# Kernel tuning notes

Hardware: AMD Instinct MI355X
Metric: run time of the kernel (lower is better)

The kernel has to match this reference:

```python
import jax, jax.numpy as jnp
import numpy as np

N_ENTRIES = 4_194_304   # total CSR entries (gene observations)
H, W = 256, 256
N_PIXELS = H * W
N_GENES = 30000
FEATURE_DIM = 64


def setup_inputs() -> dict:
    key = jax.random.key(0)
    k1, k2, k3, k4 = jax.random.split(key, 4)
    # gene id per CSR entry
    indices = jax.random.randint(k1, (N_ENTRIES,), 0, N_GENES, dtype=jnp.int64)
    # counts per entry (positive floats)
    cnts = jax.random.uniform(k2, (N_ENTRIES,), dtype=jnp.float32) * 10.0
    # CSR row pointers over pixels: sorted, starting at 0, ending at N_ENTRIES
    indptr = jnp.sort(jax.random.randint(k3, (N_PIXELS + 1,), 0, N_ENTRIES + 1, dtype=jnp.int64))
    indptr = indptr.at[0].set(0).at[-1].set(N_ENTRIES)
    # params: gamma init zeros, tokens variance_scaling(1.0,'fan_in','normal',out_axis=0)
    gamma = jnp.zeros((N_GENES,), jnp.float32)
    tokens = jax.random.normal(k4, (N_GENES, FEATURE_DIM), dtype=jnp.float32) * (1.0 / np.sqrt(FEATURE_DIM))
    return {"indices": indices, "cnts": cnts, "indptr": indptr, "gamma": gamma, "tokens": tokens}


def reference(indices, cnts, indptr, gamma, tokens):
    # SGStem with rescale=True, normalize=False (module defaults)
    n_entries = indices.shape[0]
    n_pixels = indptr.shape[0] - 1  # == H*W
    # mask padding entries beyond indptr[-1]
    valid = jnp.arange(n_entries) < indptr[-1]
    c = jnp.where(valid, cnts, 0.0)
    # rescale counts by per-gene exp(gamma)
    c = c * jnp.exp(gamma[indices])
    # CSR -> segment ids per entry
    rpt = jnp.diff(indptr)
    segms = jnp.repeat(jnp.arange(n_pixels), rpt, total_repeat_length=n_entries)
    # gather token embeddings, scale, scatter-add into pixel bins
    embeddings = tokens[indices] * c[:, None]  # (n_entries, feature_dim)
    embedding_sum = jax.ops.segment_sum(embeddings, segms, num_segments=n_pixels)
    return embedding_sum.reshape(H, W, tokens.shape[-1])
```

## Files before the change

### kernel.cpp

```cpp
#include <hip/hip_runtime.h>
#include <hip/hip_bf16.h>

#define FDIM 64
#define N_PIXELS 65536
#define WAVES_PER_BLOCK 4

__global__ __launch_bounds__(WAVES_PER_BLOCK * 64) void sgstem_kernel(
    const int* __restrict__ indices,
    const float* __restrict__ cnts,
    const int* __restrict__ indptr,
    const float* __restrict__ gamma,
    const float4* __restrict__ tokens4,
    float4* __restrict__ out4)
{
    __shared__ int2 meta[WAVES_PER_BLOCK][64];

    const int lane = threadIdx.x & 63;
    const int wave = threadIdx.x >> 6;
    const int g    = lane >> 4;
    const int fl   = lane & 15;
    const int pixel = blockIdx.x * WAVES_PER_BLOCK + wave;

    const int start = indptr[pixel];
    const int end   = indptr[pixel + 1];

    float4 acc = {0.f, 0.f, 0.f, 0.f};

    for (int base = start; base < end; base += 64) {
        const int e = base + lane;
        int   idx   = 0;
        float scale = 0.0f;
        if (e < end) {
            idx   = indices[e];
            scale = cnts[e] * __expf(gamma[idx]);
        }
        int2 mt;
        mt.x = idx;
        mt.y = __float_as_int(scale);
        meta[wave][lane] = mt;

        const int m = end - base;
        if (m >= 64) {
            #pragma unroll 8
            for (int j = 0; j < 16; ++j) {
                const int2 mm = meta[wave][j * 4 + g];
                const float s = __int_as_float(mm.y);
                const float4 t = tokens4[mm.x * 16 + fl];
                acc.x = fmaf(t.x, s, acc.x);
                acc.y = fmaf(t.y, s, acc.y);
                acc.z = fmaf(t.z, s, acc.z);
                acc.w = fmaf(t.w, s, acc.w);
            }
        } else {
            const int niter = (m + 3) >> 2;
            for (int j = 0; j < niter; ++j) {
                const int2 mm = meta[wave][j * 4 + g];
                const float s = __int_as_float(mm.y);
                const float4 t = tokens4[mm.x * 16 + fl];
                acc.x = fmaf(t.x, s, acc.x);
                acc.y = fmaf(t.y, s, acc.y);
                acc.z = fmaf(t.z, s, acc.z);
                acc.w = fmaf(t.w, s, acc.w);
            }
        }
    }

    acc.x += __shfl_xor(acc.x, 16);
    acc.y += __shfl_xor(acc.y, 16);
    acc.z += __shfl_xor(acc.z, 16);
    acc.w += __shfl_xor(acc.w, 16);
    acc.x += __shfl_xor(acc.x, 32);
    acc.y += __shfl_xor(acc.y, 32);
    acc.z += __shfl_xor(acc.z, 32);
    acc.w += __shfl_xor(acc.w, 32);

    if (g == 0) {
        out4[pixel * 16 + fl] = acc;
    }
}

extern "C" void kernel_launch(void* const* d_in, const int* in_sizes, int n_in,
                              void* d_out, int out_size, void* d_ws, size_t ws_size,
                              hipStream_t stream) {
    const int*    indices = (const int*)d_in[0];
    const float*  cnts    = (const float*)d_in[1];
    const int*    indptr  = (const int*)d_in[2];
    const float*  gamma   = (const float*)d_in[3];
    const float4* tokens4 = (const float4*)d_in[4];
    float4*       out4    = (float4*)d_out;

    const int nblocks = N_PIXELS / WAVES_PER_BLOCK;
    sgstem_kernel<<<nblocks, WAVES_PER_BLOCK * 64, 0, stream>>>(
        indices, cnts, indptr, gamma, tokens4, out4);
}
```

Baseline: 178.2 us.

## Gather bf16 token table and process several pixels per wave

Adds a pre-pass kernel that converts the fp32 token table to bf16 in workspace. The main kernel then gathers 16-byte bf16 rows (8 lanes per entry, 8 entries per wave step) instead of fp32 rows, halving gather traffic per entry. Each wave now processes 8 pixels sequentially with a wider shuffle reduction. This gives up precision in the token values and adds an extra launch, and fewer waves may reduce latency hiding.

```diff
diff --git a/kernel.cpp b/kernel.cpp
--- a/kernel.cpp
+++ b/kernel.cpp
@@ -3,79 +3,119 @@
 
 #define FDIM 64
 #define N_PIXELS 65536
+#define N_GENES 30000
 #define WAVES_PER_BLOCK 4
+#define PIX_PER_WAVE 8
 
-__global__ __launch_bounds__(WAVES_PER_BLOCK * 64) void sgstem_kernel(
+__device__ __forceinline__ unsigned short f32_to_bf16_rne(float f) {
+    unsigned int u = __float_as_uint(f);
+    u = (u + 0x7FFFu + ((u >> 16) & 1u)) >> 16;
+    return (unsigned short)u;
+}
+
+__global__ __launch_bounds__(256) void convert_tokens(
+    const float4* __restrict__ tokens4,
+    ushort4* __restrict__ tok_bf)
+{
+    const int i = blockIdx.x * blockDim.x + threadIdx.x;
+    const float4 t = tokens4[i];
+    ushort4 o;
+    o.x = f32_to_bf16_rne(t.x);
+    o.y = f32_to_bf16_rne(t.y);
+    o.z = f32_to_bf16_rne(t.z);
+    o.w = f32_to_bf16_rne(t.w);
+    tok_bf[i] = o;
+}
+
+__global__ __launch_bounds__(WAVES_PER_BLOCK * 64) void sgstem_main(
     const int* __restrict__ indices,
     const float* __restrict__ cnts,
     const int* __restrict__ indptr,
     const float* __restrict__ gamma,
-    const float4* __restrict__ tokens4,
+    const uint4* __restrict__ tok_bf,
     float4* __restrict__ out4)
 {
     __shared__ int2 meta[WAVES_PER_BLOCK][64];
 
     const int lane = threadIdx.x & 63;
     const int wave = threadIdx.x >> 6;
-    const int g    = lane >> 4;
-    const int fl   = lane & 15;
-    const int pixel = blockIdx.x * WAVES_PER_BLOCK + wave;
+    const int g    = lane >> 3;
+    const int fl   = lane & 7;
+    const int wgid = blockIdx.x * WAVES_PER_BLOCK + wave;
+    const int p0   = wgid * PIX_PER_WAVE;
 
-    const int start = indptr[pixel];
-    const int end   = indptr[pixel + 1];
+    for (int pixel = p0; pixel < p0 + PIX_PER_WAVE; ++pixel) {
+        const int start = indptr[pixel];
+        const int end   = indptr[pixel + 1];
 
-    float4 acc = {0.f, 0.f, 0.f, 0.f};
+        float a0 = 0.f, a1 = 0.f, a2 = 0.f, a3 = 0.f;
+        float a4 = 0.f, a5 = 0.f, a6 = 0.f, a7 = 0.f;
 
-    for (int base = start; base < end; base += 64) {
-        const int e = base + lane;
-        int   idx   = 0;
-        float scale = 0.0f;
-        if (e < end) {
-            idx   = indices[e];
-            scale = cnts[e] * __expf(gamma[idx]);
-        }
-        int2 mt;
-        mt.x = idx;
-        mt.y = __float_as_int(scale);
-        meta[wave][lane] = mt;
+        for (int base = start; base < end; base += 64) {
+            const int e = base + lane;
+            int   idx   = 0;
+            float scale = 0.0f;
+            if (e < end) {
+                idx   = indices[e];
+                scale = cnts[e] * __expf(gamma[idx]);
+            }
+            int2 mt;
+            mt.x = idx;
+            mt.y = __float_as_int(scale);
+            meta[wave][lane] = mt;
 
-        const int m = end - base;
-        if (m >= 64) {
-            #pragma unroll 8
-            for (int j = 0; j < 16; ++j) {
-                const int2 mm = meta[wave][j * 4 + g];
-                const float s = __int_as_float(mm.y);
-                const float4 t = tokens4[mm.x * 16 + fl];
-                acc.x = fmaf(t.x, s, acc.x);
-                acc.y = fmaf(t.y, s, acc.y);
-                acc.z = fmaf(t.z, s, acc.z);
-                acc.w = fmaf(t.w, s, acc.w);
-            }
-        } else {
-            const int niter = (m + 3) >> 2;
-            for (int j = 0; j < niter; ++j) {
-                const int2 mm = meta[wave][j * 4 + g];
-                const float s = __int_as_float(mm.y);
-                const float4 t = tokens4[mm.x * 16 + fl];
-                acc.x = fmaf(t.x, s, acc.x);
-                acc.y = fmaf(t.y, s, acc.y);
-                acc.z = fmaf(t.z, s, acc.z);
-                acc.w = fmaf(t.w, s, acc.w);
+            const int m = end - base;
+            if (m >= 64) {
+                #pragma unroll 8
+                for (int j = 0; j < 8; ++j) {
+                    const int2 mm = meta[wave][j * 8 + g];
+                    const float s = __int_as_float(mm.y);
+                    const uint4 t = tok_bf[mm.x * 8 + fl];
+                    a0 = fmaf(__uint_as_float(t.x << 16), s, a0);
+                    a1 = fmaf(__uint_as_float(t.x & 0xFFFF0000u), s, a1);
+                    a2 = fmaf(__uint_as_float(t.y << 16), s, a2);
+                    a3 = fmaf(__uint_as_float(t.y & 0xFFFF0000u), s, a3);
+                    a4 = fmaf(__uint_as_float(t.z << 16), s, a4);
+                    a5 = fmaf(__uint_as_float(t.z & 0xFFFF0000u), s, a5);
+                    a6 = fmaf(__uint_as_float(t.w << 16), s, a6);
+                    a7 = fmaf(__uint_as_float(t.w & 0xFFFF0000u), s, a7);
+                }
+            } else {
+                const int niter = (m + 7) >> 3;
+                for (int j = 0; j < niter; ++j) {
+                    const int2 mm = meta[wave][j * 8 + g];
+                    const float s = __int_as_float(mm.y);
+                    const uint4 t = tok_bf[mm.x * 8 + fl];
+                    a0 = fmaf(__uint_as_float(t.x << 16), s, a0);
+                    a1 = fmaf(__uint_as_float(t.x & 0xFFFF0000u), s, a1);
+                    a2 = fmaf(__uint_as_float(t.y << 16), s, a2);
+                    a3 = fmaf(__uint_as_float(t.y & 0xFFFF0000u), s, a3);
+                    a4 = fmaf(__uint_as_float(t.z << 16), s, a4);
+                    a5 = fmaf(__uint_as_float(t.z & 0xFFFF0000u), s, a5);
+                    a6 = fmaf(__uint_as_float(t.w << 16), s, a6);
+                    a7 = fmaf(__uint_as_float(t.w & 0xFFFF0000u), s, a7);
+                }
             }
         }
-    }
 
-    acc.x += __shfl_xor(acc.x, 16);
-    acc.y += __shfl_xor(acc.y, 16);
-    acc.z += __shfl_xor(acc.z, 16);
-    acc.w += __shfl_xor(acc.w, 16);
-    acc.x += __shfl_xor(acc.x, 32);
-    acc.y += __shfl_xor(acc.y, 32);
-    acc.z += __shfl_xor(acc.z, 32);
-    acc.w += __shfl_xor(acc.w, 32);
+        #pragma unroll
+        for (int mask = 8; mask <= 32; mask <<= 1) {
+            a0 += __shfl_xor(a0, mask);
+            a1 += __shfl_xor(a1, mask);
+            a2 += __shfl_xor(a2, mask);
+            a3 += __shfl_xor(a3, mask);
+            a4 += __shfl_xor(a4, mask);
+            a5 += __shfl_xor(a5, mask);
+            a6 += __shfl_xor(a6, mask);
+            a7 += __shfl_xor(a7, mask);
+        }
 
-    if (g == 0) {
-        out4[pixel * 16 + fl] = acc;
+        if (g == 0) {
+            float4 lo = make_float4(a0, a1, a2, a3);
+            float4 hi = make_float4(a4, a5, a6, a7);
+            out4[pixel * 16 + fl * 2]     = lo;
+            out4[pixel * 16 + fl * 2 + 1] = hi;
+        }
     }
 }
 
@@ -89,7 +129,11 @@
     const float4* tokens4 = (const float4*)d_in[4];
     float4*       out4    = (float4*)d_out;
 
-    const int nblocks = N_PIXELS / WAVES_PER_BLOCK;
-    sgstem_kernel<<<nblocks, WAVES_PER_BLOCK * 64, 0, stream>>>(
-        indices, cnts, indptr, gamma, tokens4, out4);
+    ushort4* tok_bf = (ushort4*)d_ws;
+
+    convert_tokens<<<1875, 256, 0, stream>>>(tokens4, tok_bf);
+
+    const int nblocks = N_PIXELS / (WAVES_PER_BLOCK * PIX_PER_WAVE);
+    sgstem_main<<<nblocks, WAVES_PER_BLOCK * 64, 0, stream>>>(
+        indices, cnts, indptr, gamma, (const uint4*)tok_bf, out4);
 }
```

Result: faster. 165.3 us (-7.2%).
